# Performance work log

Hardware: AMD Instinct MI355X
Metric: run time of the kernel (lower is better)

## Reference

```python
import jax, jax.numpy as jnp
import numpy as np

B, N, C = 16, 1024, 1152
H = 16
D = C // H  # 72
INNER = 4608
EPS = 1e-6


def _layernorm(x, g, b):
    mu = jnp.mean(x, axis=-1, keepdims=True)
    var = jnp.mean(jnp.square(x - mu), axis=-1, keepdims=True)
    return (x - mu) * jax.lax.rsqrt(var + EPS) * g + b


def setup_inputs() -> dict:
    key = jax.random.key(0)
    ks = jax.random.split(key, 16)
    s_c = 1.0 / np.sqrt(C)
    s_i = 1.0 / np.sqrt(INNER)
    return {
        "x": jax.random.normal(ks[0], (B, N, C), dtype=jnp.float32),
        "ln1_g": jnp.ones((C,), jnp.float32),
        "ln1_b": jnp.zeros((C,), jnp.float32),
        # weights stored (in, out) so y = x @ W + b (equiv to torch x @ W.T + b)
        "qkv_w": jax.random.normal(ks[1], (C, 3 * C), jnp.float32) * s_c,
        "qkv_b": jnp.zeros((3 * C,), jnp.float32),
        "proj_w": jax.random.normal(ks[2], (C, C), jnp.float32) * s_c,
        "proj_b": jnp.zeros((C,), jnp.float32),
        "ln2_g": jnp.ones((C,), jnp.float32),
        "ln2_b": jnp.zeros((C,), jnp.float32),
        "fc1_w": jax.random.normal(ks[3], (C, INNER), jnp.float32) * s_c,
        "fc1_b": jnp.zeros((INNER,), jnp.float32),
        "fc2_w": jax.random.normal(ks[4], (INNER, C), jnp.float32) * s_i,
        "fc2_b": jnp.zeros((C,), jnp.float32),
    }


def reference(x, ln1_g, ln1_b, qkv_w, qkv_b, proj_w, proj_b,
              ln2_g, ln2_b, fc1_w, fc1_b, fc2_w, fc2_b):
    scale = D ** -0.5
    # --- attention branch ---
    h = _layernorm(x, ln1_g, ln1_b)
    qkv = (h @ qkv_w + qkv_b).reshape(B, N, 3, H, D)
    q, k, v = jnp.moveaxis(qkv, 2, 0)            # each (B, N, H, D)
    q = q.transpose(0, 2, 1, 3)                   # (B, H, N, D)
    k = k.transpose(0, 2, 1, 3)
    v = v.transpose(0, 2, 1, 3)
    attn = jnp.einsum('bhnd,bhmd->bhnm', q, k) * scale
    attn = jax.nn.softmax(attn, axis=-1)
    out = jnp.einsum('bhnm,bhmd->bhnd', attn, v)
    out = out.transpose(0, 2, 1, 3).reshape(B, N, C)
    x = x + out @ proj_w + proj_b
    # --- MLP branch ---
    h = _layernorm(x, ln2_g, ln2_b)
    h = jax.nn.gelu(h @ fc1_w + fc1_b, approximate=False)
    x = x + h @ fc2_w + fc2_b
    return x
```

## Files before the change

### kernel.cpp

```cpp
#include <hip/hip_runtime.h>
#include <hip/hip_bf16.h>

typedef unsigned short ushort_t;
using short8 = __attribute__((ext_vector_type(8))) short;
using f32x4  = __attribute__((ext_vector_type(4))) float;

#define DEVI __device__ __forceinline__

DEVI ushort_t f2bf(float f) {
    union { float f; unsigned u; } c; c.f = f;
    unsigned u = c.u;
    return (ushort_t)((u + 0x7FFF + ((u >> 16) & 1)) >> 16);
}

DEVI f32x4 mfma16(short8 a, short8 b, f32x4 c) {
    return __builtin_amdgcn_mfma_f32_16x16x32_bf16(a, b, c, 0, 0, 0);
}

DEVI void gld16(const void* g, void* l) {
    __builtin_amdgcn_global_load_lds(
        (const __attribute__((address_space(1))) unsigned int*)g,
        (__attribute__((address_space(3))) unsigned int*)l, 16, 0, 0);
}

#define Bsz 16
#define Ntok 1024
#define Cdim 1152
#define Hn 16
#define Dh 72
#define Dp 96
#define INNER 4608
#define Mrows (Bsz * Ntok)

#define OFF_QKV_WT  ((size_t)0)
#define OFF_PROJ_WT ((size_t)8257536)
#define OFF_FC1_WT  ((size_t)11206656)
#define OFF_FC2_WT  ((size_t)21823488)
#define OFF_H       ((size_t)33619968)
#define OFF_ATT     ((size_t)71368704)
#define OFF_Q       ((size_t)109117440)
#define OFF_K       ((size_t)159449088)
#define OFF_VT      ((size_t)209780736)
#define OFF_HIDDEN  OFF_Q

__global__ __launch_bounds__(256) void transpose_cast(
    const float* __restrict__ W, ushort_t* __restrict__ Wt, int K, int N)
{
    __shared__ float t[64][65];
    const int n0 = blockIdx.x * 64;
    const int k0 = blockIdx.y * 64;
    #pragma unroll
    for (int j = 0; j < 4; ++j) {
        int idx = threadIdx.x + j * 256;
        int r = idx >> 4;
        int c4 = idx & 15;
        float4 v = *(const float4*)&W[(size_t)(k0 + r) * N + n0 + c4 * 4];
        t[r][c4 * 4 + 0] = v.x; t[r][c4 * 4 + 1] = v.y;
        t[r][c4 * 4 + 2] = v.z; t[r][c4 * 4 + 3] = v.w;
    }
    __syncthreads();
    #pragma unroll
    for (int j = 0; j < 4; ++j) {
        int idx = threadIdx.x + j * 256;
        int rn = idx >> 4;
        int c4 = idx & 15;
        ushort4 o;
        o.x = f2bf(t[c4 * 4 + 0][rn]);
        o.y = f2bf(t[c4 * 4 + 1][rn]);
        o.z = f2bf(t[c4 * 4 + 2][rn]);
        o.w = f2bf(t[c4 * 4 + 3][rn]);
        *(ushort4*)&Wt[(size_t)(n0 + rn) * K + k0 + c4 * 4] = o;
    }
}

__global__ __launch_bounds__(256) void ln_kernel(
    const float* __restrict__ x, const float* __restrict__ g,
    const float* __restrict__ b, ushort_t* __restrict__ out)
{
    const int row = blockIdx.x;
    const int tid = threadIdx.x;
    const int lane = tid & 63, wid = tid >> 6;
    const float* xr = x + (size_t)row * Cdim;

    float4 v0 = ((const float4*)xr)[tid];
    float4 v1 = {0, 0, 0, 0};
    if (tid < 32) v1 = ((const float4*)xr)[256 + tid];
    float s  = v0.x + v0.y + v0.z + v0.w + v1.x + v1.y + v1.z + v1.w;
    float s2 = v0.x*v0.x + v0.y*v0.y + v0.z*v0.z + v0.w*v0.w
             + v1.x*v1.x + v1.y*v1.y + v1.z*v1.z + v1.w*v1.w;
    #pragma unroll
    for (int off = 32; off >= 1; off >>= 1) {
        s  += __shfl_xor(s, off);
        s2 += __shfl_xor(s2, off);
    }
    __shared__ float red[8];
    if (lane == 0) { red[wid] = s; red[4 + wid] = s2; }
    __syncthreads();
    s  = red[0] + red[1] + red[2] + red[3];
    s2 = red[4] + red[5] + red[6] + red[7];
    const float mu = s * (1.0f / Cdim);
    const float var = s2 * (1.0f / Cdim) - mu * mu;
    const float rs = rsqrtf(var + 1e-6f);

    ushort_t* orow = out + (size_t)row * Cdim;
    {
        float4 g4 = ((const float4*)g)[tid];
        float4 b4 = ((const float4*)b)[tid];
        ushort4 o;
        o.x = f2bf((v0.x - mu) * rs * g4.x + b4.x);
        o.y = f2bf((v0.y - mu) * rs * g4.y + b4.y);
        o.z = f2bf((v0.z - mu) * rs * g4.z + b4.z);
        o.w = f2bf((v0.w - mu) * rs * g4.w + b4.w);
        ((ushort4*)orow)[tid] = o;
    }
    if (tid < 32) {
        float4 g4 = ((const float4*)g)[256 + tid];
        float4 b4 = ((const float4*)b)[256 + tid];
        ushort4 o;
        o.x = f2bf((v1.x - mu) * rs * g4.x + b4.x);
        o.y = f2bf((v1.y - mu) * rs * g4.y + b4.y);
        o.z = f2bf((v1.z - mu) * rs * g4.z + b4.z);
        o.w = f2bf((v1.w - mu) * rs * g4.w + b4.w);
        ((ushort4*)orow)[256 + tid] = o;
    }
}

enum { EPI_QKV = 0, EPI_PROJ = 1, EPI_FC1 = 2, EPI_FC2 = 3 };

#define TBM 256
#define TBN 128
#define TBK 64
#define BUFB 49152

template<int EPI, int N, int K>
__global__ __launch_bounds__(512, 1) void gemm_bt(
    const ushort_t* __restrict__ A, const ushort_t* __restrict__ Bt,
    const float* __restrict__ bias, const float* __restrict__ resid,
    float* __restrict__ outf, ushort_t* __restrict__ outb,
    ushort_t* __restrict__ outq, ushort_t* __restrict__ outk, ushort_t* __restrict__ outv)
{
    __shared__ ushort_t smem[3 * BUFB / 2];
    const int tid = threadIdx.x;
    const int lane = tid & 63, wid = tid >> 6;
    const int wr = wid >> 1, wc = wid & 1;
    const int fr = lane & 15, fq = lane >> 4;
    const int bid = blockIdx.x;
    constexpr int NTt = K / TBK;
    constexpr int NTN = N / TBN;
    constexpr int TT  = (Mrows / TBM) * NTN;

    size_t srcA[4]; int dstA[4];
    #pragma unroll
    for (int r = 0; r < 4; ++r) {
        const int chunk = r * 512 + tid;
        const int row = chunk >> 3, slot = chunk & 7;
        srcA[r] = (size_t)row * K + (slot ^ (row & 7)) * 8;
        dstA[r] = chunk * 16;
    }
    size_t srcB[2]; int dstB[2];
    #pragma unroll
    for (int r = 0; r < 2; ++r) {
        const int chunk = r * 512 + tid;
        const int row = chunk >> 3, slot = chunk & 7;
        srcB[r] = (size_t)row * K + (slot ^ (row & 7)) * 8;
        dstB[r] = 32768 + chunk * 16;
    }
    const int swz = (fr & 7) << 4;
    int aoff[4][2], boff[4][2];
    #pragma unroll
    for (int kh = 0; kh < 2; ++kh) {
        const int colb = (kh * 64 + fq * 16) ^ swz;
        #pragma unroll
        for (int i = 0; i < 4; ++i) {
            aoff[i][kh] = (wr * 64 + i * 16 + fr) * 128 + colb;
            boff[i][kh] = 32768 + (wc * 64 + i * 16 + fr) * 128 + colb;
        }
    }

    const int nj = (TT - bid + 255) / 256;
    const int total_u = nj * NTt;

    int js = 0, ts = 0, sbuf = 0;
    const ushort_t *sAb, *sBb;
    auto setbases = [&](int j) {
        int s = bid + j * 256; if (s >= TT) s = bid;
        const int mt = s & 63, nt = s >> 6;
        sAb = A + (size_t)(mt * TBM) * K;
        sBb = Bt + (size_t)(nt * TBN) * K;
    };
    setbases(0);
    auto STAGE = [&]() {
        char* lb = (char*)smem + (size_t)sbuf * BUFB;
        const ushort_t* Ab = sAb + ts * TBK;
        const ushort_t* Bb = sBb + ts * TBK;
        #pragma unroll
        for (int r = 0; r < 4; ++r) gld16(Ab + srcA[r], lb + dstA[r]);
        #pragma unroll
        for (int r = 0; r < 2; ++r) gld16(Bb + srcB[r], lb + dstB[r]);
        sbuf = (sbuf == 2) ? 0 : sbuf + 1;
        if (++ts == NTt) { ts = 0; setbases(++js); }
    };

    f32x4 acc[4][4] = {};
    STAGE(); STAGE();

    int jc = 0, tc = 0, cbuf = 0;
    for (int u = 0; u < total_u; ++u) {
        asm volatile("s_waitcnt vmcnt(6)" ::: "memory");
        __builtin_amdgcn_s_barrier();
        __builtin_amdgcn_sched_barrier(0);
        STAGE();
        __builtin_amdgcn_sched_barrier(0);
        const char* lb = (const char*)smem + (size_t)cbuf * BUFB;
        #pragma unroll
        for (int kh = 0; kh < 2; ++kh) {
            short8 a[4], b[4];
            #pragma unroll
            for (int i = 0; i < 4; ++i) {
                a[i] = *(const short8*)(lb + aoff[i][kh]);
                b[i] = *(const short8*)(lb + boff[i][kh]);
            }
            __builtin_amdgcn_s_setprio(1);
            #pragma unroll
            for (int mi = 0; mi < 4; ++mi)
                #pragma unroll
                for (int ni = 0; ni < 4; ++ni)
                    acc[mi][ni] = mfma16(a[mi], b[ni], acc[mi][ni]);
            __builtin_amdgcn_s_setprio(0);
        }
        cbuf = (cbuf == 2) ? 0 : cbuf + 1;

        if (++tc == NTt) {
            tc = 0;
            const int s = bid + jc * 256;
            const int m0 = (s & 63) * TBM, n0 = (s >> 6) * TBN;
            #pragma unroll
            for (int mi = 0; mi < 4; ++mi) {
                #pragma unroll
                for (int ni = 0; ni < 4; ++ni) {
                    const int col = n0 + wc * 64 + ni * 16 + fr;
                    const int rbase = m0 + wr * 64 + mi * 16 + fq * 4;
                    #pragma unroll
                    for (int i = 0; i < 4; ++i) {
                        const int r = rbase + i;
                        float v = acc[mi][ni][i];
                        if (EPI == EPI_QKV) {
                            v += bias[col];
                            const int which = col / Cdim;
                            const int rc = col % Cdim;
                            const int h = rc / Dh, d = rc % Dh;
                            const int b2 = r >> 10, n = r & 1023;
                            const size_t head = (size_t)(b2 * Hn + h);
                            if (which == 0)      outq[(head * Ntok + n) * Dp + d] = f2bf(v);
                            else if (which == 1) outk[(head * Ntok + n) * Dp + d] = f2bf(v);
                            else                 outv[(head * Dp + d) * Ntok + n] = f2bf(v);
                        } else if (EPI == EPI_PROJ) {
                            v += bias[col] + resid[(size_t)r * N + col];
                            outf[(size_t)r * N + col] = v;
                        } else if (EPI == EPI_FC1) {
                            v += bias[col];
                            v = 0.5f * v * (1.0f + erff(v * 0.70710678118f));
                            outb[(size_t)r * N + col] = f2bf(v);
                        } else {
                            v += bias[col] + outf[(size_t)r * N + col];
                            outf[(size_t)r * N + col] = v;
                        }
                        acc[mi][ni][i] = 0.0f;
                    }
                }
            }
            ++jc;
        }
    }
}

__global__ __launch_bounds__(256) void attn_kernel(
    const ushort_t* __restrict__ q, const ushort_t* __restrict__ k,
    const ushort_t* __restrict__ vt, ushort_t* __restrict__ out)
{
    const int tid = threadIdx.x;
    const int lane = tid & 63, wid = tid >> 6;
    const int bid = blockIdx.x;
    const int xcd = bid & 7;
    const int bh = (bid >> 6) * 8 + xcd;
    const int qblk = (bid >> 3) & 7;
    const int qbase = qblk * 128 + wid * 32;
    const int fr = lane & 15, fq = lane >> 4;
    const ushort_t* qh = q  + (size_t)bh * Ntok * Dp;
    const ushort_t* kh = k  + (size_t)bh * Ntok * Dp;
    const ushort_t* vh = vt + (size_t)bh * Dp * Ntok;

    short8 aq[2][3];
    #pragma unroll
    for (int t = 0; t < 2; ++t)
        #pragma unroll
        for (int ks = 0; ks < 3; ++ks)
            aq[t][ks] = *(const short8*)&qh[(size_t)(qbase + t * 16 + fr) * Dp + ks * 32 + fq * 8];

    f32x4 o[2][5] = {};
    float lsum[2][4] = {};

    __shared__ ushort_t plds[4][2][16][32];
    const float scale = 0.117851130f;

    for (int kv = 0; kv < Ntok; kv += 32) {
        short8 kb0[3], kb1[3], bv[5];
        #pragma unroll
        for (int ks = 0; ks < 3; ++ks) {
            kb0[ks] = *(const short8*)&kh[(size_t)(kv + fr) * Dp + ks * 32 + fq * 8];
            kb1[ks] = *(const short8*)&kh[(size_t)(kv + 16 + fr) * Dp + ks * 32 + fq * 8];
        }
        #pragma unroll
        for (int dt = 0; dt < 5; ++dt)
            bv[dt] = *(const short8*)&vh[(size_t)(dt * 16 + fr) * Ntok + kv + fq * 8];

        f32x4 s[2][2] = {};
        __builtin_amdgcn_s_setprio(1);
        #pragma unroll
        for (int ks = 0; ks < 3; ++ks)
            #pragma unroll
            for (int t = 0; t < 2; ++t) {
                s[t][0] = mfma16(aq[t][ks], kb0[ks], s[t][0]);
                s[t][1] = mfma16(aq[t][ks], kb1[ks], s[t][1]);
            }
        __builtin_amdgcn_s_setprio(0);

        #pragma unroll
        for (int t = 0; t < 2; ++t) {
            #pragma unroll
            for (int i = 0; i < 4; ++i) {
                float p0 = __expf(s[t][0][i] * scale);
                float p1 = __expf(s[t][1][i] * scale);
                lsum[t][i] += p0 + p1;
                plds[wid][t][fq * 4 + i][fr]      = f2bf(p0);
                plds[wid][t][fq * 4 + i][16 + fr] = f2bf(p1);
            }
        }
        short8 pa[2];
        #pragma unroll
        for (int t = 0; t < 2; ++t)
            pa[t] = *(const short8*)&plds[wid][t][fr][fq * 8];
        __builtin_amdgcn_s_setprio(1);
        #pragma unroll
        for (int dt = 0; dt < 5; ++dt)
            #pragma unroll
            for (int t = 0; t < 2; ++t)
                o[t][dt] = mfma16(pa[t], bv[dt], o[t][dt]);
        __builtin_amdgcn_s_setprio(0);
    }

    const int b = bh >> 4, h = bh & 15;
    #pragma unroll
    for (int t = 0; t < 2; ++t) {
        float inv[4];
        #pragma unroll
        for (int i = 0; i < 4; ++i) {
            float s = lsum[t][i];
            s += __shfl_xor(s, 1);
            s += __shfl_xor(s, 2);
            s += __shfl_xor(s, 4);
            s += __shfl_xor(s, 8);
            inv[i] = 1.0f / s;
        }
        #pragma unroll
        for (int dt = 0; dt < 5; ++dt) {
            const int d = dt * 16 + fr;
            if (d < Dh) {
                #pragma unroll
                for (int i = 0; i < 4; ++i) {
                    const size_t idx = ((size_t)(b * Ntok) + qbase + t * 16 + fq * 4 + i) * Cdim + h * Dh + d;
                    out[idx] = f2bf(o[t][dt][i] * inv[i]);
                }
            }
        }
    }
}

extern "C" void kernel_launch(void* const* d_in, const int* in_sizes, int n_in,
                              void* d_out, int out_size, void* d_ws, size_t ws_size,
                              hipStream_t stream) {
    const float* x      = (const float*)d_in[0];
    const float* ln1_g  = (const float*)d_in[1];
    const float* ln1_b  = (const float*)d_in[2];
    const float* qkv_w  = (const float*)d_in[3];
    const float* qkv_b  = (const float*)d_in[4];
    const float* proj_w = (const float*)d_in[5];
    const float* proj_b = (const float*)d_in[6];
    const float* ln2_g  = (const float*)d_in[7];
    const float* ln2_b  = (const float*)d_in[8];
    const float* fc1_w  = (const float*)d_in[9];
    const float* fc1_b  = (const float*)d_in[10];
    const float* fc2_w  = (const float*)d_in[11];
    const float* fc2_b  = (const float*)d_in[12];

    char* ws = (char*)d_ws;
    ushort_t* qkv_wT  = (ushort_t*)(ws + OFF_QKV_WT);
    ushort_t* proj_wT = (ushort_t*)(ws + OFF_PROJ_WT);
    ushort_t* fc1_wT  = (ushort_t*)(ws + OFF_FC1_WT);
    ushort_t* fc2_wT  = (ushort_t*)(ws + OFF_FC2_WT);
    ushort_t* hbuf    = (ushort_t*)(ws + OFF_H);
    ushort_t* attnout = (ushort_t*)(ws + OFF_ATT);
    ushort_t* qb      = (ushort_t*)(ws + OFF_Q);
    ushort_t* kb      = (ushort_t*)(ws + OFF_K);
    ushort_t* vtb     = (ushort_t*)(ws + OFF_VT);
    ushort_t* hidden  = (ushort_t*)(ws + OFF_HIDDEN);
    float* out = (float*)d_out;

    hipMemsetAsync(ws + OFF_Q, 0, (size_t)3 * 50331648, stream);

    transpose_cast<<<dim3(3 * Cdim / 64, Cdim / 64), 256, 0, stream>>>(qkv_w, qkv_wT, Cdim, 3 * Cdim);
    transpose_cast<<<dim3(Cdim / 64, Cdim / 64), 256, 0, stream>>>(proj_w, proj_wT, Cdim, Cdim);
    transpose_cast<<<dim3(INNER / 64, Cdim / 64), 256, 0, stream>>>(fc1_w, fc1_wT, Cdim, INNER);
    transpose_cast<<<dim3(Cdim / 64, INNER / 64), 256, 0, stream>>>(fc2_w, fc2_wT, INNER, Cdim);

    ln_kernel<<<Mrows, 256, 0, stream>>>(x, ln1_g, ln1_b, hbuf);

    gemm_bt<EPI_QKV, 3 * Cdim, Cdim><<<256, 512, 0, stream>>>(
        hbuf, qkv_wT, qkv_b, nullptr, nullptr, nullptr, qb, kb, vtb);

    attn_kernel<<<2048, 256, 0, stream>>>(qb, kb, vtb, attnout);

    gemm_bt<EPI_PROJ, Cdim, Cdim><<<256, 512, 0, stream>>>(
        attnout, proj_wT, proj_b, x, out, nullptr, nullptr, nullptr, nullptr);

    ln_kernel<<<Mrows, 256, 0, stream>>>(out, ln2_g, ln2_b, hbuf);

    gemm_bt<EPI_FC1, INNER, Cdim><<<256, 512, 0, stream>>>(
        hbuf, fc1_wT, fc1_b, nullptr, nullptr, hidden, nullptr, nullptr, nullptr);

    gemm_bt<EPI_FC2, Cdim, INNER><<<256, 512, 0, stream>>>(
        hidden, fc2_wT, fc2_b, nullptr, out, nullptr, nullptr, nullptr, nullptr);
}
```

Baseline: 1.056 ms.

## Software-pipeline K/V register loads in attention loop and pad P LDS tile

Unrolls the attention KV loop by two and double-buffers K and V fragments in registers, so the loads for the next 32-key chunk are issued before the MFMAs of the current chunk. The aim is to hide global-load latency behind compute. It also pads the per-wave P staging buffer rows from 32 to 40 elements to reduce LDS bank conflicts. In exchange the kernel holds more live VGPRs, which may lower occupancy.

```diff
diff --git a/kernel.cpp b/kernel.cpp
--- a/kernel.cpp
+++ b/kernel.cpp
@@ -300,54 +300,76 @@
     f32x4 o[2][5] = {};
     float lsum[2][4] = {};
 
-    __shared__ ushort_t plds[4][2][16][32];
+    __shared__ ushort_t plds[4][2][16][40];
     const float scale = 0.117851130f;
 
-    for (int kv = 0; kv < Ntok; kv += 32) {
-        short8 kb0[3], kb1[3], bv[5];
+    short8 kA0[3], kA1[3], kB0[3], kB1[3], v0[5], v1[5];
+    #pragma unroll
+    for (int ks = 0; ks < 3; ++ks) {
+        kA0[ks] = *(const short8*)&kh[(size_t)(fr) * Dp + ks * 32 + fq * 8];
+        kA1[ks] = *(const short8*)&kh[(size_t)(16 + fr) * Dp + ks * 32 + fq * 8];
+    }
+
+    #define ATTN_HALF(KB0, KB1, VV, KVOFF)                                            \
+    {                                                                                 \
+        f32x4 s[2][2] = {};                                                           \
+        __builtin_amdgcn_s_setprio(1);                                                \
+        _Pragma("unroll")                                                             \
+        for (int ks = 0; ks < 3; ++ks)                                                \
+            _Pragma("unroll")                                                         \
+            for (int t = 0; t < 2; ++t) {                                             \
+                s[t][0] = mfma16(aq[t][ks], KB0[ks], s[t][0]);                        \
+                s[t][1] = mfma16(aq[t][ks], KB1[ks], s[t][1]);                        \
+            }                                                                         \
+        __builtin_amdgcn_s_setprio(0);                                                \
+        _Pragma("unroll")                                                             \
+        for (int t = 0; t < 2; ++t) {                                                 \
+            _Pragma("unroll")                                                         \
+            for (int i = 0; i < 4; ++i) {                                             \
+                float p0 = __expf(s[t][0][i] * scale);                                \
+                float p1 = __expf(s[t][1][i] * scale);                                \
+                lsum[t][i] += p0 + p1;                                                \
+                plds[wid][t][fq * 4 + i][fr]      = f2bf(p0);                         \
+                plds[wid][t][fq * 4 + i][16 + fr] = f2bf(p1);                         \
+            }                                                                         \
+        }                                                                             \
+        short8 pa[2];                                                                 \
+        _Pragma("unroll")                                                             \
+        for (int t = 0; t < 2; ++t)                                                   \
+            pa[t] = *(const short8*)&plds[wid][t][fr][fq * 8];                        \
+        __builtin_amdgcn_s_setprio(1);                                                \
+        _Pragma("unroll")                                                             \
+        for (int dt = 0; dt < 5; ++dt)                                                \
+            _Pragma("unroll")                                                         \
+            for (int t = 0; t < 2; ++t)                                               \
+                o[t][dt] = mfma16(pa[t], VV[dt], o[t][dt]);                           \
+        __builtin_amdgcn_s_setprio(0);                                                \
+    }
+
+    for (int kv = 0; kv < Ntok; kv += 64) {
+        #pragma unroll
+        for (int dt = 0; dt < 5; ++dt)
+            v0[dt] = *(const short8*)&vh[(size_t)(dt * 16 + fr) * Ntok + kv + fq * 8];
         #pragma unroll
         for (int ks = 0; ks < 3; ++ks) {
-            kb0[ks] = *(const short8*)&kh[(size_t)(kv + fr) * Dp + ks * 32 + fq * 8];
-            kb1[ks] = *(const short8*)&kh[(size_t)(kv + 16 + fr) * Dp + ks * 32 + fq * 8];
-        }
+            kB0[ks] = *(const short8*)&kh[(size_t)(kv + 32 + fr) * Dp + ks * 32 + fq * 8];
+            kB1[ks] = *(const short8*)&kh[(size_t)(kv + 48 + fr) * Dp + ks * 32 + fq * 8];
+        }
+        ATTN_HALF(kA0, kA1, v0, kv)
+
         #pragma unroll
         for (int dt = 0; dt < 5; ++dt)
-            bv[dt] = *(const short8*)&vh[(size_t)(dt * 16 + fr) * Ntok + kv + fq * 8];
-
-        f32x4 s[2][2] = {};
-        __builtin_amdgcn_s_setprio(1);
-        #pragma unroll
-        for (int ks = 0; ks < 3; ++ks)
+            v1[dt] = *(const short8*)&vh[(size_t)(dt * 16 + fr) * Ntok + kv + 32 + fq * 8];
+        if (kv + 64 < Ntok) {
             #pragma unroll
-            for (int t = 0; t < 2; ++t) {
-                s[t][0] = mfma16(aq[t][ks], kb0[ks], s[t][0]);
-                s[t][1] = mfma16(aq[t][ks], kb1[ks], s[t][1]);
+            for (int ks = 0; ks < 3; ++ks) {
+                kA0[ks] = *(const short8*)&kh[(size_t)(kv + 64 + fr) * Dp + ks * 32 + fq * 8];
+                kA1[ks] = *(const short8*)&kh[(size_t)(kv + 80 + fr) * Dp + ks * 32 + fq * 8];
             }
-        __builtin_amdgcn_s_setprio(0);
-
-        #pragma unroll
-        for (int t = 0; t < 2; ++t) {
-            #pragma unroll
-            for (int i = 0; i < 4; ++i) {
-                float p0 = __expf(s[t][0][i] * scale);
-                float p1 = __expf(s[t][1][i] * scale);
-                lsum[t][i] += p0 + p1;
-                plds[wid][t][fq * 4 + i][fr]      = f2bf(p0);
-                plds[wid][t][fq * 4 + i][16 + fr] = f2bf(p1);
-            }
-        }
-        short8 pa[2];
-        #pragma unroll
-        for (int t = 0; t < 2; ++t)
-            pa[t] = *(const short8*)&plds[wid][t][fr][fq * 8];
-        __builtin_amdgcn_s_setprio(1);
-        #pragma unroll
-        for (int dt = 0; dt < 5; ++dt)
-            #pragma unroll
-            for (int t = 0; t < 2; ++t)
-                o[t][dt] = mfma16(pa[t], bv[dt], o[t][dt]);
-        __builtin_amdgcn_s_setprio(0);
-    }
+        }
+        ATTN_HALF(kB0, kB1, v1, kv + 32)
+    }
+    #undef ATTN_HALF
 
     const int b = bh >> 4, h = bh & 15;
     #pragma unroll
```

Measured after the change: 1.060 ms. About the same (+0.4%).
